# Performance work log

Measured on AMD Instinct MI355X. Metric: run time of the kernel, lower is better.

Reference implementation:

```python
import math
import jax, jax.numpy as jnp
import numpy as np

B, N, D, H = 16, 256, 1024, 16
DK = D // H
LAM_ATT, LAM_DIST = 0.33, 0.33
LAM_ADJ = 1.0 - LAM_ATT - LAM_DIST
EPS, NEG_INF = 1e-6, 1e12


def setup_inputs() -> dict:
    key = jax.random.key(0)
    ks = jax.random.split(key, 16)
    inp = {
        'query': jax.random.normal(ks[0], (B, N, D), jnp.float32),
        'key': jax.random.normal(ks[1], (B, N, D), jnp.float32),
        'value': jax.random.normal(ks[2], (B, N, D), jnp.float32),
        'adj_matrix': jax.random.uniform(ks[3], (B, N, N), jnp.float32),
        'distance_matrix': jax.random.uniform(ks[4], (B, N, N), jnp.float32),
        'edges_att': jnp.zeros((1,), jnp.float32),  # unused by forward
    }
    mask = jax.random.randint(ks[5], (B, N), 0, 2, jnp.int32)
    inp['mask'] = mask.at[:, 0].set(1)  # guarantee >=1 valid atom per graph
    scale = 0.02
    inp['Wq'] = jax.random.normal(ks[6], (D, D), jnp.float32) * scale
    inp['bq'] = jnp.zeros((D,), jnp.float32)
    inp['Wk'] = jax.random.normal(ks[7], (D, D), jnp.float32) * scale
    inp['bk'] = jnp.zeros((D,), jnp.float32)
    inp['Wv'] = jax.random.normal(ks[8], (D, D), jnp.float32) * scale
    inp['bv'] = jnp.zeros((D,), jnp.float32)
    inp['Wo'] = jax.random.normal(ks[9], (D, D), jnp.float32) * scale
    inp['bo'] = jnp.zeros((D,), jnp.float32)
    return inp


def reference(query, key, value, adj_matrix, distance_matrix, edges_att, mask,
              Wq, bq, Wk, bk, Wv, bv, Wo, bo):
    b, n, d = query.shape
    proj = lambda x, W, bias: (x @ W + bias).reshape(b, n, H, DK).transpose(0, 2, 1, 3)
    q = proj(query, Wq, bq)   # [B,H,N,DK]
    k = proj(key, Wk, bk)
    v = proj(value, Wv, bv)

    scores = jnp.einsum('bhqd,bhkd->bhqk', q, k) / math.sqrt(DK)
    key_invalid = (mask == 0)[:, None, None, :]          # [B,1,1,N]
    scores = jnp.where(key_invalid, -NEG_INF, scores)
    p_attn = jax.nn.softmax(scores, axis=-1)             # [B,H,N,N]

    # row-normalized adjacency (broadcast over heads instead of repeat)
    p_adj = adj_matrix / (adj_matrix.sum(axis=-1, keepdims=True) + EPS)  # [B,N,N]

    # distance kernel: softmax(-dist) with masked columns sent to +inf
    dist = jnp.where((mask == 0)[:, None, :], jnp.inf, distance_matrix)  # [B,N,N]
    p_dist = jax.nn.softmax(-dist, axis=-1)

    p_weighted = (LAM_ATT * p_attn
                  + LAM_DIST * p_dist[:, None]
                  + LAM_ADJ * p_adj[:, None])            # [B,H,N,N]
    # dropout p=0.0 -> identity

    x = jnp.einsum('bhqk,bhkd->bhqd', p_weighted, v)     # [B,H,N,DK]
    x = x.transpose(0, 2, 1, 3).reshape(b, n, d)
    return x @ Wo + bo
```

## Files before the change

### kernel.cpp

```cpp
#include <hip/hip_runtime.h>
#include <hip/hip_bf16.h>

typedef short short8 __attribute__((ext_vector_type(8)));
typedef float floatx4 __attribute__((ext_vector_type(4)));

constexpr int BB  = 16;
constexpr int NN  = 256;
constexpr int DD  = 1024;
constexpr int HHc = 16;
constexpr int DKc = 64;

constexpr float LAM_ATT  = 0.33f;
constexpr float LAM_DIST = 0.33f;
constexpr float LAM_ADJ  = 0.34f;
constexpr float EPS_     = 1e-6f;

__device__ __forceinline__ float loadf(const void* p, size_t i, int f32) {
    return f32 ? ((const float*)p)[i] : (float)((const __hip_bfloat16*)p)[i];
}

__device__ __forceinline__ short8 load8_bf16(const void* p, size_t i, int f32) {
    if (f32) {
        const float4* q = (const float4*)((const float*)p + i);
        float4 a = q[0], b = q[1];
        short8 r;
        r[0] = (short)__bfloat16_as_ushort(__float2bfloat16(a.x));
        r[1] = (short)__bfloat16_as_ushort(__float2bfloat16(a.y));
        r[2] = (short)__bfloat16_as_ushort(__float2bfloat16(a.z));
        r[3] = (short)__bfloat16_as_ushort(__float2bfloat16(a.w));
        r[4] = (short)__bfloat16_as_ushort(__float2bfloat16(b.x));
        r[5] = (short)__bfloat16_as_ushort(__float2bfloat16(b.y));
        r[6] = (short)__bfloat16_as_ushort(__float2bfloat16(b.z));
        r[7] = (short)__bfloat16_as_ushort(__float2bfloat16(b.w));
        return r;
    }
    return *(const short8*)((const __hip_bfloat16*)p + i);
}

__device__ __forceinline__ void gl_lds16(const void* g, void* l) {
    __builtin_amdgcn_global_load_lds(
        (const __attribute__((address_space(1))) void*)g,
        (__attribute__((address_space(3))) void*)l, 16, 0, 0);
}

__global__ __launch_bounds__(256) void detect_kernel(
    const void* __restrict__ query, const void* __restrict__ maskraw,
    int* __restrict__ mask_canon, int* __restrict__ flags)
{
    __shared__ int s_f32;
    const int tid = threadIdx.x;
    if (tid == 0) s_f32 = 0;
    __syncthreads();

    const unsigned short* qh = (const unsigned short*)query;
    int hit = 0;
    for (int i = tid; i < 16384; i += 256)
        if ((qh[i] & 0x7F80u) == 0x7F80u) hit = 1;
    if (hit) atomicOr(&s_f32, 1);
    __syncthreads();
    if (tid == 0) flags[0] = s_f32;

    unsigned int w0 = ((const unsigned int*)maskraw)[0];
    int mdt = (w0 == 1u) ? 0 : ((w0 == 0x3F800000u) ? 1 : 2);

    for (int i = tid; i < BB * NN; i += 256) {
        int v;
        if (mdt == 0)      v = (((const int*)maskraw)[i] != 0);
        else if (mdt == 1) v = ((((const unsigned int*)maskraw)[i] & 0x7FFFFFFFu) != 0u);
        else               v = ((((const unsigned short*)maskraw)[i] & 0x7FFFu) != 0);
        mask_canon[i] = v;
    }
}

__global__ __launch_bounds__(256) void prep_w(
    const void* W0, const void* W1, const void* W2, const void* W3,
    const int* __restrict__ flags, __hip_bfloat16* __restrict__ Wt_all)
{
    const int f32 = flags[0];
    const void* W = (blockIdx.z == 0) ? W0 : (blockIdx.z == 1) ? W1
                  : (blockIdx.z == 2) ? W2 : W3;
    __hip_bfloat16* Wt = Wt_all + (size_t)blockIdx.z * DD * DD;
    __shared__ __hip_bfloat16 T[64][66];
    const int k0 = blockIdx.y * 64, n0 = blockIdx.x * 64;
    #pragma unroll
    for (int i = 0; i < 16; i++) {
        int e = threadIdx.x + i * 256;
        int kr = e >> 6, nc = e & 63;
        T[kr][nc] = __float2bfloat16(loadf(W, (size_t)(k0 + kr) * DD + n0 + nc, f32));
    }
    __syncthreads();
    #pragma unroll
    for (int i = 0; i < 16; i++) {
        int e = threadIdx.x + i * 256;
        int nr = e >> 6, kc = e & 63;
        Wt[(size_t)(n0 + nr) * DD + k0 + kc] = T[kc][nr];
    }
}

__global__ __launch_bounds__(256) void prep_bias(
    const void* b0, const void* b1, const void* b2, const void* b3,
    const int* __restrict__ flags, __hip_bfloat16* __restrict__ bias_all)
{
    const int f32 = flags[0];
    const void* s = (blockIdx.x == 0) ? b0 : (blockIdx.x == 1) ? b1
                  : (blockIdx.x == 2) ? b2 : b3;
    #pragma unroll
    for (int i = 0; i < 4; i++) {
        int idx = threadIdx.x + i * 256;
        bias_all[blockIdx.x * DD + idx] = __float2bfloat16(loadf(s, idx, f32));
    }
}

__global__ __launch_bounds__(256) void mix_kernel(
    const void* __restrict__ adj, const void* __restrict__ dist,
    const int* __restrict__ mask_canon, const int* __restrict__ flags,
    __hip_bfloat16* __restrict__ Mmix)
{
    const int f32 = flags[0];
    const int wave = threadIdx.x >> 6, lane = threadIdx.x & 63;
    const int b = blockIdx.y;
    const int q = blockIdx.x * 4 + wave;
    const size_t rowOff = ((size_t)b * NN + q) * NN;
    const int c0 = lane * 4;

    float a[4], nd[4];
    int msk[4];
    #pragma unroll
    for (int i = 0; i < 4; i++) {
        a[i]   = loadf(adj, rowOff + c0 + i, f32);
        msk[i] = mask_canon[b * NN + c0 + i];
        nd[i]  = msk[i] ? -loadf(dist, rowOff + c0 + i, f32) : -3.0e38f;
    }

    float asum = a[0] + a[1] + a[2] + a[3];
    #pragma unroll
    for (int off = 1; off < 64; off <<= 1) asum += __shfl_xor(asum, off);

    float mx = fmaxf(fmaxf(nd[0], nd[1]), fmaxf(nd[2], nd[3]));
    #pragma unroll
    for (int off = 1; off < 64; off <<= 1) mx = fmaxf(mx, __shfl_xor(mx, off));

    float e[4];
    float esum = 0.f;
    #pragma unroll
    for (int i = 0; i < 4; i++) {
        e[i] = msk[i] ? __expf(nd[i] - mx) : 0.f;
        esum += e[i];
    }
    #pragma unroll
    for (int off = 1; off < 64; off <<= 1) esum += __shfl_xor(esum, off);

    const float ia = 1.f / (asum + EPS_);
    const float ie = 1.f / fmaxf(esum, 1e-30f);
    __hip_bfloat16 out[4];
    #pragma unroll
    for (int i = 0; i < 4; i++)
        out[i] = __float2bfloat16(LAM_DIST * e[i] * ie + LAM_ADJ * a[i] * ia);
    *(short4*)((unsigned short*)Mmix + rowOff + c0) = *(short4*)out;
}

__device__ __forceinline__ void gemm_core(
    const void* __restrict__ A,
    const __hip_bfloat16* __restrict__ Wt,
    const __hip_bfloat16* __restrict__ bias,
    void* __restrict__ C,
    int a_f32, int c_f32, int rowBase, int colBase)
{
    __shared__ __hip_bfloat16 As[128][32];
    __shared__ __hip_bfloat16 Ws[128][32];

    const int tid  = threadIdx.x;
    const int wave = tid >> 6, lane = tid & 63;
    const int quad = lane >> 4, cl = lane & 15;
    const int wm = (wave >> 1) * 64, wn = (wave & 1) * 64;
    const int lr = lane >> 2;
    const int lc = (lane & 3) * 8;

    floatx4 acc[4][4];
    #pragma unroll
    for (int i = 0; i < 4; i++)
        #pragma unroll
        for (int j = 0; j < 4; j++)
            acc[i][j] = (floatx4){0.f, 0.f, 0.f, 0.f};

    for (int k0 = 0; k0 < DD; k0 += 32) {
        if (!a_f32) {
            #pragma unroll
            for (int j = 0; j < 2; j++) {
                int r0 = (wave * 2 + j) * 16;
                gl_lds16((const __hip_bfloat16*)A +
                             (size_t)(rowBase + r0 + lr) * DD + k0 + lc,
                         &As[r0][0]);
            }
        } else {
            #pragma unroll
            for (int i = 0; i < 2; i++) {
                int c = tid + i * 256;
                int r = c >> 2, kg = (c & 3) * 8;
                *(short8*)&As[r][kg] =
                    load8_bf16(A, (size_t)(rowBase + r) * DD + k0 + kg, 1);
            }
        }
        #pragma unroll
        for (int j = 0; j < 2; j++) {
            int r0 = (wave * 2 + j) * 16;
            gl_lds16(Wt + (size_t)(colBase + r0 + lr) * DD + k0 + lc, &Ws[r0][0]);
        }
        __syncthreads();

        short8 af[4], bfr[4];
        #pragma unroll
        for (int ms = 0; ms < 4; ms++)
            af[ms] = *(const short8*)&As[wm + ms * 16 + cl][quad * 8];
        #pragma unroll
        for (int ns = 0; ns < 4; ns++)
            bfr[ns] = *(const short8*)&Ws[wn + ns * 16 + cl][quad * 8];
        #pragma unroll
        for (int ms = 0; ms < 4; ms++)
            #pragma unroll
            for (int ns = 0; ns < 4; ns++)
                acc[ms][ns] = __builtin_amdgcn_mfma_f32_16x16x32_bf16(
                    af[ms], bfr[ns], acc[ms][ns], 0, 0, 0);
        __syncthreads();
    }

    #pragma unroll
    for (int ns = 0; ns < 4; ns++) {
        int col = colBase + wn + ns * 16 + cl;
        float bc = (float)bias[col];
        #pragma unroll
        for (int ms = 0; ms < 4; ms++) {
            #pragma unroll
            for (int r = 0; r < 4; r++) {
                int row = rowBase + wm + ms * 16 + quad * 4 + r;
                float v = acc[ms][ns][r] + bc;
                size_t idx = (size_t)row * DD + col;
                if (c_f32) ((float*)C)[idx] = v;
                else ((__hip_bfloat16*)C)[idx] = __float2bfloat16(v);
            }
        }
    }
}

__global__ __launch_bounds__(256) void qkv_mfma(
    const void* q, const void* k, const void* v,
    const __hip_bfloat16* __restrict__ Wt_all,
    const __hip_bfloat16* __restrict__ bias_all,
    __hip_bfloat16* Qp, __hip_bfloat16* Kp, __hip_bfloat16* Vp,
    const int* __restrict__ flags)
{
    const int z = blockIdx.z;
    const void* A = (z == 0) ? q : (z == 1) ? k : v;
    __hip_bfloat16* C = (z == 0) ? Qp : (z == 1) ? Kp : Vp;
    gemm_core(A, Wt_all + (size_t)z * DD * DD, bias_all + z * DD, C,
              flags[0], 0, blockIdx.y * 128, blockIdx.x * 128);
}

__global__ __launch_bounds__(256) void out_mfma(
    const __hip_bfloat16* __restrict__ X,
    const __hip_bfloat16* __restrict__ Wt,
    const __hip_bfloat16* __restrict__ bias,
    void* C, const int* __restrict__ flags)
{
    gemm_core(X, Wt, bias, C, 0, flags[0], blockIdx.y * 128, blockIdx.x * 128);
}

__global__ __launch_bounds__(256) void transpose_v(
    const __hip_bfloat16* __restrict__ Vp, __hip_bfloat16* __restrict__ Vt)
{
    __shared__ __hip_bfloat16 T[256][66];
    const int h = blockIdx.x, b = blockIdx.y;
    const int tid = threadIdx.x;
    #pragma unroll 8
    for (int i = 0; i < 64; i++) {
        int e = tid + i * 256;
        int tok = e >> 6, dk = e & 63;
        T[tok][dk] = Vp[((size_t)(b * NN + tok)) * DD + h * DKc + dk];
    }
    __syncthreads();
    #pragma unroll 8
    for (int i = 0; i < 64; i++) {
        int e = tid + i * 256;
        int dk = e >> 8, tok = e & 255;
        Vt[((size_t)((b * HHc + h) * DKc + dk)) * NN + tok] = T[tok][dk];
    }
}

__global__ __launch_bounds__(256) void attn_mfma(
    const __hip_bfloat16* __restrict__ Qp,
    const __hip_bfloat16* __restrict__ Kp,
    const __hip_bfloat16* __restrict__ Vt,
    const __hip_bfloat16* __restrict__ Mmix,
    const int* __restrict__ mask_canon,
    __hip_bfloat16* __restrict__ X)
{
    __shared__ __hip_bfloat16 Ps[4][16][264];

    const int qt = blockIdx.x, h = blockIdx.y, b = blockIdx.z;
    const int tid = threadIdx.x;
    const int wave = tid >> 6, lane = tid & 63;
    const int quad = lane >> 4, cl = lane & 15;
    const int q0 = qt * 64 + wave * 16;

    const size_t qoff = ((size_t)(b * NN + q0 + cl)) * DD + h * DKc + quad * 8;
    short8 aq0 = *(const short8*)(Qp + qoff);
    short8 aq1 = *(const short8*)(Qp + qoff + 32);

    int msk[16];
    #pragma unroll
    for (int ns = 0; ns < 16; ns++)
        msk[ns] = mask_canon[b * NN + ns * 16 + cl];

    floatx4 accS[16];
    #pragma unroll
    for (int ns = 0; ns < 16; ns++) accS[ns] = (floatx4){0.f, 0.f, 0.f, 0.f};
    #pragma unroll
    for (int ns = 0; ns < 16; ns++) {
        const size_t koff = ((size_t)(b * NN + ns * 16 + cl)) * DD + h * DKc + quad * 8;
        short8 bk0 = *(const short8*)(Kp + koff);
        short8 bk1 = *(const short8*)(Kp + koff + 32);
        accS[ns] = __builtin_amdgcn_mfma_f32_16x16x32_bf16(aq0, bk0, accS[ns], 0, 0, 0);
        accS[ns] = __builtin_amdgcn_mfma_f32_16x16x32_bf16(aq1, bk1, accS[ns], 0, 0, 0);
    }

    #pragma unroll
    for (int r = 0; r < 4; r++) {
        float s[16];
        #pragma unroll
        for (int ns = 0; ns < 16; ns++)
            s[ns] = msk[ns] ? accS[ns][r] * 0.125f : -1e12f;
        float mx = s[0];
        #pragma unroll
        for (int ns = 1; ns < 16; ns++) mx = fmaxf(mx, s[ns]);
        mx = fmaxf(mx, __shfl_xor(mx, 1));
        mx = fmaxf(mx, __shfl_xor(mx, 2));
        mx = fmaxf(mx, __shfl_xor(mx, 4));
        mx = fmaxf(mx, __shfl_xor(mx, 8));
        float e[16], sum = 0.f;
        #pragma unroll
        for (int ns = 0; ns < 16; ns++) {
            e[ns] = msk[ns] ? __expf(s[ns] - mx) : 0.f;
            sum += e[ns];
        }
        sum += __shfl_xor(sum, 1);
        sum += __shfl_xor(sum, 2);
        sum += __shfl_xor(sum, 4);
        sum += __shfl_xor(sum, 8);
        float inv = LAM_ATT / sum;
        const size_t mrow = ((size_t)b * NN + q0 + quad * 4 + r) * NN;
        #pragma unroll
        for (int ns = 0; ns < 16; ns++) {
            float p = e[ns] * inv + (float)Mmix[mrow + ns * 16 + cl];
            Ps[wave][quad * 4 + r][ns * 16 + cl] = __float2bfloat16(p);
        }
    }
    __syncthreads();

    floatx4 accX[4];
    #pragma unroll
    for (int nd = 0; nd < 4; nd++) accX[nd] = (floatx4){0.f, 0.f, 0.f, 0.f};
    #pragma unroll
    for (int ks = 0; ks < 8; ks++) {
        short8 ap = *(const short8*)&Ps[wave][cl][ks * 32 + quad * 8];
        #pragma unroll
        for (int nd = 0; nd < 4; nd++) {
            const size_t voff = ((size_t)((b * HHc + h) * DKc + nd * 16 + cl)) * NN
                              + ks * 32 + quad * 8;
            short8 bv = *(const short8*)(Vt + voff);
            accX[nd] = __builtin_amdgcn_mfma_f32_16x16x32_bf16(ap, bv, accX[nd], 0, 0, 0);
        }
    }
    #pragma unroll
    for (int nd = 0; nd < 4; nd++) {
        #pragma unroll
        for (int r = 0; r < 4; r++) {
            int row = b * NN + q0 + quad * 4 + r;
            X[(size_t)row * DD + h * DKc + nd * 16 + cl] = __float2bfloat16(accX[nd][r]);
        }
    }
}

extern "C" void kernel_launch(void* const* d_in, const int* in_sizes, int n_in,
                              void* d_out, int out_size, void* d_ws, size_t ws_size,
                              hipStream_t stream)
{
    const void* query   = d_in[0];
    const void* key     = d_in[1];
    const void* value   = d_in[2];
    const void* adj     = d_in[3];
    const void* dist    = d_in[4];
    const void* maskraw = d_in[6];
    const void* Wq = d_in[7];   const void* bq = d_in[8];
    const void* Wk = d_in[9];   const void* bk = d_in[10];
    const void* Wv = d_in[11];  const void* bv = d_in[12];
    const void* Wo = d_in[13];  const void* bo = d_in[14];

    char* w = (char*)d_ws;
    int* mask_canon = (int*)w;
    int* flags      = (int*)(w + 16384);
    __hip_bfloat16* Wt_all   = (__hip_bfloat16*)(w + 32768);
    __hip_bfloat16* bias_all = (__hip_bfloat16*)(w + 32768 + ((size_t)8 << 20));
    char* base2 = w + 32768 + ((size_t)8 << 20) + 32768;
    const size_t tokElems = (size_t)BB * NN * DD;
    __hip_bfloat16* Qp   = (__hip_bfloat16*)base2;
    __hip_bfloat16* Kp   = Qp + tokElems;
    __hip_bfloat16* Vp   = Kp + tokElems;
    __hip_bfloat16* Vt   = Vp + tokElems;
    __hip_bfloat16* Mmix = Vt + tokElems;

    detect_kernel<<<1, 256, 0, stream>>>(query, maskraw, mask_canon, flags);
    prep_w<<<dim3(16, 16, 4), 256, 0, stream>>>(Wq, Wk, Wv, Wo, flags, Wt_all);
    prep_bias<<<dim3(4), 256, 0, stream>>>(bq, bk, bv, bo, flags, bias_all);
    mix_kernel<<<dim3(NN / 4, BB), 256, 0, stream>>>(adj, dist, mask_canon, flags, Mmix);

    qkv_mfma<<<dim3(8, 32, 3), 256, 0, stream>>>(query, key, value,
                                                 Wt_all, bias_all, Qp, Kp, Vp, flags);

    transpose_v<<<dim3(HHc, BB), 256, 0, stream>>>(Vp, Vt);

    attn_mfma<<<dim3(4, HHc, BB), 256, 0, stream>>>(Qp, Kp, Vt, Mmix, mask_canon, Vp);

    out_mfma<<<dim3(8, 32), 256, 0, stream>>>(Vp, Wt_all + (size_t)3 * DD * DD,
                                              bias_all + 3 * DD, d_out, flags);
}
```

Measured before the change: 297.0 us.

## Fuse V transpose into QKV epilogue, remap blocks per XCD, shrink out-proj tiles

The V projection epilogue now writes directly in the transposed [b,h,dk,tok] layout, so the separate transpose_v kernel and its extra global round trip are gone. The QKV, attention and output GEMM launches switch to 1D grids whose block index is decoded so that neighbouring tiles land on the same XCD, which is meant to improve L2 reuse of shared operands. The output projection uses 128x64 tiles to double its block count (512) for better CU occupancy. The cost is scattered 8-byte Vt stores in the epilogue and more A-tile reloads in the output GEMM.

```diff
diff --git a/kernel.cpp b/kernel.cpp
--- a/kernel.cpp
+++ b/kernel.cpp
@@ -2,6 +2,7 @@
 #include <hip/hip_bf16.h>
 
 typedef short short8 __attribute__((ext_vector_type(8)));
+typedef short short4v __attribute__((ext_vector_type(4)));
 typedef float floatx4 __attribute__((ext_vector_type(4)));
 
 constexpr int BB  = 16;
@@ -156,45 +157,48 @@
     #pragma unroll
     for (int i = 0; i < 4; i++)
         out[i] = __float2bfloat16(LAM_DIST * e[i] * ie + LAM_ADJ * a[i] * ia);
-    *(short4*)((unsigned short*)Mmix + rowOff + c0) = *(short4*)out;
-}
-
+    *(short4v*)((unsigned short*)Mmix + rowOff + c0) = *(short4v*)out;
+}
+
+template<int MSUB, int NSUB>
 __device__ __forceinline__ void gemm_core(
     const void* __restrict__ A,
     const __hip_bfloat16* __restrict__ Wt,
     const __hip_bfloat16* __restrict__ bias,
     void* __restrict__ C,
-    int a_f32, int c_f32, int rowBase, int colBase)
-{
-    __shared__ __hip_bfloat16 As[128][32];
-    __shared__ __hip_bfloat16 Ws[128][32];
+    int a_f32, int c_f32, int rowBase, int colBase,
+    __hip_bfloat16* __restrict__ Vt, int writeVt)
+{
+    constexpr int BM = 32 * MSUB, BN = 32 * NSUB;
+    __shared__ __hip_bfloat16 As[BM][32];
+    __shared__ __hip_bfloat16 Ws[BN][32];
 
     const int tid  = threadIdx.x;
     const int wave = tid >> 6, lane = tid & 63;
     const int quad = lane >> 4, cl = lane & 15;
-    const int wm = (wave >> 1) * 64, wn = (wave & 1) * 64;
+    const int wm = (wave >> 1) * (16 * MSUB), wn = (wave & 1) * (16 * NSUB);
     const int lr = lane >> 2;
     const int lc = (lane & 3) * 8;
 
-    floatx4 acc[4][4];
-    #pragma unroll
-    for (int i = 0; i < 4; i++)
-        #pragma unroll
-        for (int j = 0; j < 4; j++)
+    floatx4 acc[MSUB][NSUB];
+    #pragma unroll
+    for (int i = 0; i < MSUB; i++)
+        #pragma unroll
+        for (int j = 0; j < NSUB; j++)
             acc[i][j] = (floatx4){0.f, 0.f, 0.f, 0.f};
 
     for (int k0 = 0; k0 < DD; k0 += 32) {
         if (!a_f32) {
             #pragma unroll
-            for (int j = 0; j < 2; j++) {
-                int r0 = (wave * 2 + j) * 16;
+            for (int j = 0; j < MSUB / 2; j++) {
+                int r0 = (wave * (MSUB / 2) + j) * 16;
                 gl_lds16((const __hip_bfloat16*)A +
                              (size_t)(rowBase + r0 + lr) * DD + k0 + lc,
                          &As[r0][0]);
             }
         } else {
             #pragma unroll
-            for (int i = 0; i < 2; i++) {
+            for (int i = 0; i < BM / 64; i++) {
                 int c = tid + i * 256;
                 int r = c >> 2, kg = (c & 3) * 8;
                 *(short8*)&As[r][kg] =
@@ -202,41 +206,56 @@
             }
         }
         #pragma unroll
-        for (int j = 0; j < 2; j++) {
-            int r0 = (wave * 2 + j) * 16;
+        for (int j = 0; j < NSUB / 2; j++) {
+            int r0 = (wave * (NSUB / 2) + j) * 16;
             gl_lds16(Wt + (size_t)(colBase + r0 + lr) * DD + k0 + lc, &Ws[r0][0]);
         }
         __syncthreads();
 
-        short8 af[4], bfr[4];
-        #pragma unroll
-        for (int ms = 0; ms < 4; ms++)
+        short8 af[MSUB], bfr[NSUB];
+        #pragma unroll
+        for (int ms = 0; ms < MSUB; ms++)
             af[ms] = *(const short8*)&As[wm + ms * 16 + cl][quad * 8];
         #pragma unroll
-        for (int ns = 0; ns < 4; ns++)
+        for (int ns = 0; ns < NSUB; ns++)
             bfr[ns] = *(const short8*)&Ws[wn + ns * 16 + cl][quad * 8];
         #pragma unroll
-        for (int ms = 0; ms < 4; ms++)
+        for (int ms = 0; ms < MSUB; ms++)
             #pragma unroll
-            for (int ns = 0; ns < 4; ns++)
+            for (int ns = 0; ns < NSUB; ns++)
                 acc[ms][ns] = __builtin_amdgcn_mfma_f32_16x16x32_bf16(
                     af[ms], bfr[ns], acc[ms][ns], 0, 0, 0);
         __syncthreads();
     }
 
     #pragma unroll
-    for (int ns = 0; ns < 4; ns++) {
+    for (int ns = 0; ns < NSUB; ns++) {
         int col = colBase + wn + ns * 16 + cl;
         float bc = (float)bias[col];
-        #pragma unroll
-        for (int ms = 0; ms < 4; ms++) {
+        if (writeVt) {
+            int h = col >> 6, dk = col & 63;
             #pragma unroll
-            for (int r = 0; r < 4; r++) {
-                int row = rowBase + wm + ms * 16 + quad * 4 + r;
-                float v = acc[ms][ns][r] + bc;
-                size_t idx = (size_t)row * DD + col;
-                if (c_f32) ((float*)C)[idx] = v;
-                else ((__hip_bfloat16*)C)[idx] = __float2bfloat16(v);
+            for (int ms = 0; ms < MSUB; ms++) {
+                int row0 = rowBase + wm + ms * 16 + quad * 4;
+                int b = row0 >> 8, tok = row0 & 255;
+                __hip_bfloat16 pk[4];
+                #pragma unroll
+                for (int r = 0; r < 4; r++)
+                    pk[r] = __float2bfloat16(acc[ms][ns][r] + bc);
+                *(short4v*)&Vt[((size_t)((b * HHc + h) * DKc + dk)) * NN + tok] =
+                    *(short4v*)pk;
+            }
+        } else {
+            #pragma unroll
+            for (int ms = 0; ms < MSUB; ms++) {
+                #pragma unroll
+                for (int r = 0; r < 4; r++) {
+                    int row = rowBase + wm + ms * 16 + quad * 4 + r;
+                    float v = acc[ms][ns][r] + bc;
+                    size_t idx = (size_t)row * DD + col;
+                    if (c_f32) ((float*)C)[idx] = v;
+                    else ((__hip_bfloat16*)C)[idx] = __float2bfloat16(v);
+                }
             }
         }
     }
@@ -246,14 +265,20 @@
     const void* q, const void* k, const void* v,
     const __hip_bfloat16* __restrict__ Wt_all,
     const __hip_bfloat16* __restrict__ bias_all,
-    __hip_bfloat16* Qp, __hip_bfloat16* Kp, __hip_bfloat16* Vp,
+    __hip_bfloat16* Qp, __hip_bfloat16* Kp, __hip_bfloat16* Vt,
     const int* __restrict__ flags)
 {
-    const int z = blockIdx.z;
+    const int bid = blockIdx.x;
+    const int xcd = bid & 7, s = bid >> 3;
+    const int x = s & 7;
+    const int t = s >> 3;
+    const int y = xcd + 8 * (t & 3);
+    const int z = t >> 2;
+
     const void* A = (z == 0) ? q : (z == 1) ? k : v;
-    __hip_bfloat16* C = (z == 0) ? Qp : (z == 1) ? Kp : Vp;
-    gemm_core(A, Wt_all + (size_t)z * DD * DD, bias_all + z * DD, C,
-              flags[0], 0, blockIdx.y * 128, blockIdx.x * 128);
+    __hip_bfloat16* C = (z == 0) ? Qp : Kp;
+    gemm_core<4, 4>(A, Wt_all + (size_t)z * DD * DD, bias_all + z * DD, C,
+                    flags[0], 0, y * 128, x * 128, Vt, z == 2);
 }
 
 __global__ __launch_bounds__(256) void out_mfma(
@@ -262,28 +287,11 @@
     const __hip_bfloat16* __restrict__ bias,
     void* C, const int* __restrict__ flags)
 {
-    gemm_core(X, Wt, bias, C, 0, flags[0], blockIdx.y * 128, blockIdx.x * 128);
-}
-
-__global__ __launch_bounds__(256) void transpose_v(
-    const __hip_bfloat16* __restrict__ Vp, __hip_bfloat16* __restrict__ Vt)
-{
-    __shared__ __hip_bfloat16 T[256][66];
-    const int h = blockIdx.x, b = blockIdx.y;
-    const int tid = threadIdx.x;
-    #pragma unroll 8
-    for (int i = 0; i < 64; i++) {
-        int e = tid + i * 256;
-        int tok = e >> 6, dk = e & 63;
-        T[tok][dk] = Vp[((size_t)(b * NN + tok)) * DD + h * DKc + dk];
-    }
-    __syncthreads();
-    #pragma unroll 8
-    for (int i = 0; i < 64; i++) {
-        int e = tid + i * 256;
-        int dk = e >> 8, tok = e & 255;
-        Vt[((size_t)((b * HHc + h) * DKc + dk)) * NN + tok] = T[tok][dk];
-    }
+    const int bid = blockIdx.x;
+    const int xcd = bid & 7, s = bid >> 3;
+    const int x = s & 15;
+    const int y = xcd + 8 * (s >> 4);
+    gemm_core<4, 2>(X, Wt, bias, C, 0, flags[0], y * 128, x * 64, nullptr, 0);
 }
 
 __global__ __launch_bounds__(256) void attn_mfma(
@@ -296,7 +304,12 @@
 {
     __shared__ __hip_bfloat16 Ps[4][16][264];
 
-    const int qt = blockIdx.x, h = blockIdx.y, b = blockIdx.z;
+    const int bid = blockIdx.x;
+    const int xcd = bid & 7, sdec = bid >> 3;
+    const int qt = sdec & 3;
+    const int hb = xcd + 8 * (sdec >> 2);
+    const int h = hb & 15, b = hb >> 4;
+
     const int tid = threadIdx.x;
     const int wave = tid >> 6, lane = tid & 63;
     const int quad = lane >> 4, cl = lane & 15;
@@ -404,8 +417,8 @@
     const size_t tokElems = (size_t)BB * NN * DD;
     __hip_bfloat16* Qp   = (__hip_bfloat16*)base2;
     __hip_bfloat16* Kp   = Qp + tokElems;
-    __hip_bfloat16* Vp   = Kp + tokElems;
-    __hip_bfloat16* Vt   = Vp + tokElems;
+    __hip_bfloat16* X    = Kp + tokElems;
+    __hip_bfloat16* Vt   = X  + tokElems;
     __hip_bfloat16* Mmix = Vt + tokElems;
 
     detect_kernel<<<1, 256, 0, stream>>>(query, maskraw, mask_canon, flags);
@@ -413,13 +426,11 @@
     prep_bias<<<dim3(4), 256, 0, stream>>>(bq, bk, bv, bo, flags, bias_all);
     mix_kernel<<<dim3(NN / 4, BB), 256, 0, stream>>>(adj, dist, mask_canon, flags, Mmix);
 
-    qkv_mfma<<<dim3(8, 32, 3), 256, 0, stream>>>(query, key, value,
-                                                 Wt_all, bias_all, Qp, Kp, Vp, flags);
-
-    transpose_v<<<dim3(HHc, BB), 256, 0, stream>>>(Vp, Vt);
-
-    attn_mfma<<<dim3(4, HHc, BB), 256, 0, stream>>>(Qp, Kp, Vt, Mmix, mask_canon, Vp);
-
-    out_mfma<<<dim3(8, 32), 256, 0, stream>>>(Vp, Wt_all + (size_t)3 * DD * DD,
-                                              bias_all + 3 * DD, d_out, flags);
-}
+    qkv_mfma<<<768, 256, 0, stream>>>(query, key, value,
+                                      Wt_all, bias_all, Qp, Kp, Vt, flags);
+
+    attn_mfma<<<1024, 256, 0, stream>>>(Qp, Kp, Vt, Mmix, mask_canon, X);
+
+    out_mfma<<<512, 256, 0, stream>>>(X, Wt_all + (size_t)3 * DD * DD,
+                                      bias_all + 3 * DD, d_out, flags);
+}
```

Measured after the change: 278.4 us. 1.07x faster.
